# Performance work log

Hardware: AMD Instinct MI355X
Metric: run time of the kernel (lower is better)

The kernel has to match this reference:

```python
import jax, jax.numpy as jnp
import numpy as np

EPS_LN1 = 1e-6   # partial(nn.LayerNorm, eps=1e-6)
EPS_OUT = 1e-5   # nn.LayerNorm default inside SS3D out_norm


def _layernorm(x, w, b, eps):
    m = jnp.mean(x, axis=-1, keepdims=True)
    v = jnp.var(x, axis=-1, keepdims=True)
    return (x - m) * jax.lax.rsqrt(v + eps) * w + b


def _selective_scan(dA, dBx):
    # dA, dBx: (B, K, d, L, N); linear recurrence h_t = dA_t * h_{t-1} + dBx_t
    def comb(c1, c2):
        a1, b1 = c1
        a2, b2 = c2
        return a2 * a1, a2 * b1 + b2
    _, hs = jax.lax.associative_scan(comb, (dA, dBx), axis=3)
    return hs  # (B, K, d, L, N)


def setup_inputs() -> dict:
    key = jax.random.key(0)
    ks = jax.random.split(key, 12)
    B, D, H, W, C = 1, 16, 16, 16, 96
    d, N, K, R = 96, 16, 6, 6  # d_inner, d_state, n_scan_dirs, dt_rank
    s = 0.02
    f = lambda k, shp: jax.random.normal(k, shp, dtype=jnp.float32)
    return {
        "x": f(ks[0], (B, D, H, W, C)),
        "ln1_w": jnp.ones((C,), jnp.float32),
        "ln1_b": jnp.zeros((C,), jnp.float32),
        "in_proj_w": f(ks[1], (2 * d, C)) * s,
        "conv_w": f(ks[2], (d, 1, 3, 3, 3)) * s,
        "conv_b": f(ks[3], (d,)) * s,
        "x_proj_w": f(ks[4], (K, R + 2 * N, d)) * s,
        "dt_proj_w": f(ks[5], (K, d, R)) * s,
        "dt_proj_b": f(ks[6], (K, d)) * s,
        "A_log": jnp.log(1.0 + 15.0 * jax.random.uniform(ks[7], (K, d, N), jnp.float32)),
        "D_skip": f(ks[8], (K, d)) * s,
        "out_norm_w": jnp.ones((d,), jnp.float32),
        "out_norm_b": jnp.zeros((d,), jnp.float32),
        "out_proj_w": f(ks[9], (C, d)) * s,
    }


def reference(x, ln1_w, ln1_b, in_proj_w, conv_w, conv_b, x_proj_w,
              dt_proj_w, dt_proj_b, A_log, D_skip, out_norm_w, out_norm_b,
              out_proj_w):
    B, D, H, W, C = x.shape
    L = D * H * W
    K, _, d = x_proj_w.shape
    R = dt_proj_w.shape[2]
    N = A_log.shape[2]

    # pre-norm
    xn = _layernorm(x, ln1_w, ln1_b, EPS_LN1)

    # in_proj -> (x, z)
    xz = jnp.einsum('bdhwc,ec->bdhwe', xn, in_proj_w)  # (B,D,H,W,2d)
    xh, z = jnp.split(xz, 2, axis=-1)

    # depthwise 3x3x3 conv + SiLU, channels-first
    xc = jnp.transpose(xh, (0, 4, 1, 2, 3))  # (B,d,D,H,W)
    xc = jax.lax.conv_general_dilated(
        xc, conv_w, window_strides=(1, 1, 1), padding='SAME',
        dimension_numbers=('NCDHW', 'OIDHW', 'NCDHW'),
        feature_group_count=d)
    xc = jax.nn.silu(xc + conv_b[None, :, None, None, None])

    # K = 6 scan orderings: DHW, HWD, WDH and their reverses
    o0 = xc.reshape(B, d, L)
    o1 = jnp.transpose(xc, (0, 1, 3, 4, 2)).reshape(B, d, L)  # (H,W,D) order
    o2 = jnp.transpose(xc, (0, 1, 4, 2, 3)).reshape(B, d, L)  # (W,D,H) order
    fwd3 = jnp.stack([o0, o1, o2], axis=1)                    # (B,3,d,L)
    xs = jnp.concatenate([fwd3, jnp.flip(fwd3, axis=-1)], axis=1)  # (B,K,d,L)

    # per-direction input-dependent parameters
    x_dbl = jnp.einsum('bkdl,kcd->bkcl', xs, x_proj_w)        # (B,K,R+2N,L)
    dt, Bm, Cm = jnp.split(x_dbl, [R, R + N], axis=2)
    dts = jnp.einsum('bkrl,kdr->bkdl', dt, dt_proj_w) + dt_proj_b[None, :, :, None]
    dts = jax.nn.softplus(dts)                                # delta_softplus

    A = -jnp.exp(A_log)                                       # (K,d,N)
    dA = jnp.exp(dts[..., None] * A[None, :, :, None, :])     # (B,K,d,L,N)
    Bt = jnp.transpose(Bm, (0, 1, 3, 2))                      # (B,K,L,N)
    dBx = (dts * xs)[..., None] * Bt[:, :, None, :, :]        # (B,K,d,L,N)

    hs = _selective_scan(dA, dBx)                             # (B,K,d,L,N)
    Ct = jnp.transpose(Cm, (0, 1, 3, 2))                      # (B,K,L,N)
    ys = jnp.einsum('bkdln,bkln->bkdl', hs, Ct) + D_skip[None, :, :, None] * xs

    # undo reversals and orderings, sum the 6 paths
    yf = ys[:, :3] + jnp.flip(ys[:, 3:], axis=-1)             # (B,3,d,L)
    y0 = yf[:, 0]
    y1 = jnp.transpose(yf[:, 1].reshape(B, d, H, W, D), (0, 1, 4, 2, 3)).reshape(B, d, L)
    y2 = jnp.transpose(yf[:, 2].reshape(B, d, W, D, H), (0, 1, 3, 4, 2)).reshape(B, d, L)
    y = (y0 + y1 + y2).reshape(B, d, D, H, W)
    y = jnp.transpose(y, (0, 2, 3, 4, 1))                     # (B,D,H,W,d)

    # out_norm, gate, out_proj
    y = _layernorm(y, out_norm_w, out_norm_b, EPS_OUT)
    y = y * jax.nn.silu(z)
    out = jnp.einsum('bdhwe,ce->bdhwc', y, out_proj_w)

    # residual (drop_path is identity at eval)
    return x + out
```

## Files before the change

kernel.cpp:

```cpp
#include <hip/hip_runtime.h>
#include <hip/hip_bf16.h>

#define L 4096
#define CDIM 96
#define DDIM 96
#define KDIR 6
#define NST 16
#define RRK 6
#define YH 32
#define NCHUNK 256
#define CHLEN 16

typedef _Float16 half4v __attribute__((ext_vector_type(4)));

__device__ __forceinline__ float sigmoidf_(float x) { return 1.f / (1.f + __expf(-x)); }

__device__ __forceinline__ int sigma_k(int kb, int l) {
    if (kb == 0) return l;
    if (kb == 1) return ((l & 15) << 8) | ((l >> 8) << 4) | ((l >> 4) & 15);
    return (((l >> 4) & 15) << 8) | ((l & 15) << 4) | (l >> 8);
}

__device__ __forceinline__ int lrow_k(int k, int s) {
    int kb = (k < 3) ? k : (k - 3);
    int l;
    if (kb == 0) l = s;
    else if (kb == 1) l = sigma_k(2, s);
    else l = sigma_k(1, s);
    return (k >= 3) ? (4095 - l) : l;
}

__global__ void __launch_bounds__(192) k1_ln_inproj(
        const float* __restrict__ x, const float* __restrict__ ln_w,
        const float* __restrict__ ln_b, const float* __restrict__ Wp,
        _Float16* __restrict__ xhh, _Float16* __restrict__ zsh) {
    int s0 = blockIdx.x * 8;
    int tid = threadIdx.x;
    __shared__ __align__(16) float xt[8][96];
    __shared__ __align__(16) float xn[8][96];
    __shared__ float mss[8], rss[8];
    ((float4*)&xt[0][0])[tid] = ((const float4*)(x + (size_t)s0 * 96))[tid];
    __syncthreads();
    int wave = tid >> 6, lane = tid & 63;
    for (int r = wave; r < 8; r += 3) {
        float v = xt[r][lane] + ((lane < 32) ? xt[r][64 + lane] : 0.f);
#pragma unroll
        for (int off = 1; off < 64; off <<= 1) v += __shfl_xor(v, off);
        float vs = xt[r][lane] * xt[r][lane] + ((lane < 32) ? xt[r][64 + lane] * xt[r][64 + lane] : 0.f);
#pragma unroll
        for (int off = 1; off < 64; off <<= 1) vs += __shfl_xor(vs, off);
        if (lane == 0) {
            float mean = v * (1.f / 96.f);
            float var = vs * (1.f / 96.f) - mean * mean;
            mss[r] = mean; rss[r] = rsqrtf(var + 1e-6f);
        }
    }
    __syncthreads();
    {
        int r = tid / 24, c4 = tid % 24;
        float4 xv = ((float4*)&xt[r][0])[c4];
        float4 wv = ((const float4*)ln_w)[c4];
        float4 bv = ((const float4*)ln_b)[c4];
        float m = mss[r], rs = rss[r];
        float4 o;
        o.x = (xv.x - m) * rs * wv.x + bv.x;
        o.y = (xv.y - m) * rs * wv.y + bv.y;
        o.z = (xv.z - m) * rs * wv.z + bv.z;
        o.w = (xv.w - m) * rs * wv.w + bv.w;
        ((float4*)&xn[r][0])[c4] = o;
    }
    float4 Wr[24];
    const float4* wr = (const float4*)(Wp + (size_t)tid * 96);
#pragma unroll
    for (int c4 = 0; c4 < 24; c4++) Wr[c4] = wr[c4];
    __syncthreads();
#pragma unroll
    for (int s = 0; s < 8; s++) {
        const float4* xr4 = (const float4*)&xn[s][0];
        float a0 = 0.f, a1 = 0.f, a2 = 0.f, a3 = 0.f;
#pragma unroll
        for (int c4 = 0; c4 < 24; c4 += 4) {
            float4 x0 = xr4[c4], x1 = xr4[c4 + 1], x2 = xr4[c4 + 2], x3 = xr4[c4 + 3];
            a0 += Wr[c4].x * x0.x + Wr[c4].y * x0.y + Wr[c4].z * x0.z + Wr[c4].w * x0.w;
            a1 += Wr[c4+1].x * x1.x + Wr[c4+1].y * x1.y + Wr[c4+1].z * x1.z + Wr[c4+1].w * x1.w;
            a2 += Wr[c4+2].x * x2.x + Wr[c4+2].y * x2.y + Wr[c4+2].z * x2.z + Wr[c4+2].w * x2.w;
            a3 += Wr[c4+3].x * x3.x + Wr[c4+3].y * x3.y + Wr[c4+3].z * x3.z + Wr[c4+3].w * x3.w;
        }
        float acc = (a0 + a1) + (a2 + a3);
        if (tid < 96) xhh[(size_t)tid * L + s0 + s] = (_Float16)acc;
        else zsh[(size_t)(s0 + s) * 96 + (tid - 96)] = (_Float16)(acc * sigmoidf_(acc));
    }
}

__global__ void k2_conv(const _Float16* __restrict__ xhh, const float* __restrict__ cw,
                        const float* __restrict__ cb, _Float16* __restrict__ xch,
                        _Float16* __restrict__ xcTh) {
    int idx = blockIdx.x * 256 + threadIdx.x;
    int c = idx >> 12, s = idx & 4095;
    int dz = s >> 8, h = (s >> 4) & 15, w = s & 15;
    const _Float16* xin = xhh + (size_t)c * L;
    const float* wc = cw + c * 27;
    float acc = cb[c];
#pragma unroll
    for (int i = 0; i < 3; i++) {
        int z2 = dz + i - 1; if ((unsigned)z2 > 15u) continue;
#pragma unroll
        for (int j = 0; j < 3; j++) {
            int h2 = h + j - 1; if ((unsigned)h2 > 15u) continue;
#pragma unroll
            for (int kk = 0; kk < 3; kk++) {
                int w2 = w + kk - 1; if ((unsigned)w2 > 15u) continue;
                acc += (float)xin[z2 * 256 + h2 * 16 + w2] * wc[i * 9 + j * 3 + kk];
            }
        }
    }
    float r = acc * sigmoidf_(acc);
    _Float16 hr = (_Float16)r;
    xch[(size_t)c * L + s] = hr;
    xcTh[(size_t)s * 96 + c] = hr;
}

__global__ void k3_xproj(const _Float16* __restrict__ xch, const float* __restrict__ Wx,
                         const float* __restrict__ Wdt, const float* __restrict__ bdt,
                         _Float16* __restrict__ Yl, _Float16* __restrict__ Zl,
                         _Float16* __restrict__ dtxl) {
    int k = blockIdx.x;
    int tid = threadIdx.x;
    int sbase = blockIdx.y * 256;
    int s = sbase + tid;
    int g = blockIdx.z;
    __shared__ float dts[256][6];
    __shared__ _Float16 xcs[96][258];
    float acc[14];
#pragma unroll
    for (int i = 0; i < 14; i++) acc[i] = 0.f;
    const float* wdt_rows = Wx + (size_t)k * 38 * DDIM;
    const float* wbc      = Wx + ((size_t)k * 38 + 6 + g * 8) * DDIM;
    for (int dd = 0; dd < 96; dd += 4) {
        float v[4];
#pragma unroll
        for (int j = 0; j < 4; j++) {
            _Float16 hv = xch[(size_t)(dd + j) * L + s];
            v[j] = (float)hv;
            xcs[dd + j][tid] = hv;
        }
#pragma unroll
        for (int j = 0; j < 4; j++) {
#pragma unroll
            for (int r = 0; r < 6; r++) acc[r] += wdt_rows[r * DDIM + dd + j] * v[j];
#pragma unroll
            for (int i = 0; i < 8; i++) acc[6 + i] += wbc[i * DDIM + dd + j] * v[j];
        }
    }
    {
        int lr = lrow_k(k, s);
        _Float16* yo = Yl + ((size_t)k * L + lr) * YH;
#pragma unroll
        for (int i = 0; i < 8; i++) yo[g * 8 + i] = (_Float16)acc[6 + i];
    }
#pragma unroll
    for (int r = 0; r < 6; r++) dts[tid][r] = acc[r];
    __syncthreads();
    for (int i = 0; i < 24; i++) {
        int idx = i * 256 + tid;
        int dl = idx % 24;
        int sr = idx / 24;
        int d = g * 24 + dl;
        const float* wr = Wdt + ((size_t)k * 96 + d) * 6;
        float a = bdt[k * 96 + d];
#pragma unroll
        for (int r = 0; r < 6; r++) a += wr[r] * dts[sr][r];
        float sp = (a > 15.f) ? a : __logf(1.f + __expf(a));
        int lr = lrow_k(k, sbase + sr);
        size_t o = ((size_t)k * L + lr) * 96 + d;
        Zl[o] = (_Float16)sp;
        dtxl[o] = (_Float16)(sp * (float)xcs[d][sr]);
    }
}

__global__ void __launch_bounds__(256) ka_scan(
        const _Float16* __restrict__ Zl, const _Float16* __restrict__ dtxl,
        const _Float16* __restrict__ Yl, const float* __restrict__ A_log,
        _Float16* __restrict__ Aah, _Float16* __restrict__ Abh) {
    int t = blockIdx.x * 256 + threadIdx.x;
    int nq = t & 3;
    int q = t >> 2;
    int d = q % 96;
    int rest = q / 96;
    int chunk = rest % NCHUNK;
    int k = rest / NCHUNK;
    float An[4];
    {
        float4 al = *(const float4*)(A_log + ((size_t)k * 96 + d) * 16 + nq * 4);
        An[0] = -__expf(al.x) * 1.44269504f; An[1] = -__expf(al.y) * 1.44269504f;
        An[2] = -__expf(al.z) * 1.44269504f; An[3] = -__expf(al.w) * 1.44269504f;
    }
    float a[4] = {1.f, 1.f, 1.f, 1.f};
    float b[4] = {0.f, 0.f, 0.f, 0.f};
    const _Float16* Zk = Zl + (size_t)k * L * 96;
    const _Float16* Xk = dtxl + (size_t)k * L * 96;
    const _Float16* Yk = Yl + (size_t)k * L * YH;
    int l0 = chunk * CHLEN;
    for (int i = 0; i < CHLEN; i += 4) {
        float dt[4], dx[4]; half4v Bh[4];
#pragma unroll
        for (int j = 0; j < 4; j++) {
            int l = l0 + i + j;
            dt[j] = (float)Zk[(size_t)l * 96 + d];
            dx[j] = (float)Xk[(size_t)l * 96 + d];
            Bh[j] = *(const half4v*)(Yk + (size_t)l * YH + nq * 4);
        }
#pragma unroll
        for (int j = 0; j < 4; j++) {
            float e0 = exp2f(dt[j] * An[0]);
            float e1 = exp2f(dt[j] * An[1]);
            float e2 = exp2f(dt[j] * An[2]);
            float e3 = exp2f(dt[j] * An[3]);
            b[0] = e0 * b[0] + dx[j] * (float)Bh[j].x; a[0] *= e0;
            b[1] = e1 * b[1] + dx[j] * (float)Bh[j].y; a[1] *= e1;
            b[2] = e2 * b[2] + dx[j] * (float)Bh[j].z; a[2] *= e2;
            b[3] = e3 * b[3] + dx[j] * (float)Bh[j].w; a[3] *= e3;
        }
    }
    size_t o = (((size_t)k * NCHUNK + chunk) * 96 + d) * 16 + nq * 4;
    half4v ha, hb;
    ha.x = (_Float16)a[0]; ha.y = (_Float16)a[1]; ha.z = (_Float16)a[2]; ha.w = (_Float16)a[3];
    hb.x = (_Float16)b[0]; hb.y = (_Float16)b[1]; hb.z = (_Float16)b[2]; hb.w = (_Float16)b[3];
    *(half4v*)(Aah + o) = ha;
    *(half4v*)(Abh + o) = hb;
}

__global__ void __launch_bounds__(256) kb_combine(
        const _Float16* __restrict__ Aah, const _Float16* __restrict__ Abh,
        _Float16* __restrict__ Pbh) {
    int t = blockIdx.x * 256 + threadIdx.x;
    int n = t & 15;
    int rest = t >> 4;
    int d = rest % 96;
    int k = rest / 96;
    size_t base = ((size_t)k * NCHUNK * 96 + d) * 16 + n;
    const size_t cstride = 96 * 16;
    float rb = 0.f;
    for (int c0 = 0; c0 < NCHUNK; c0 += 16) {
        float av[16], bv[16];
#pragma unroll
        for (int j = 0; j < 16; j++) {
            av[j] = (float)Aah[base + (size_t)(c0 + j) * cstride];
            bv[j] = (float)Abh[base + (size_t)(c0 + j) * cstride];
        }
#pragma unroll
        for (int j = 0; j < 16; j++) {
            Pbh[base + (size_t)(c0 + j) * cstride] = (_Float16)rb;
            rb = av[j] * rb + bv[j];
        }
    }
}

__global__ void __launch_bounds__(256) kc_apply(
        const _Float16* __restrict__ Zl, const _Float16* __restrict__ dtxl,
        const _Float16* __restrict__ Yl, const float* __restrict__ A_log,
        const _Float16* __restrict__ Pbh, _Float16* __restrict__ ysh) {
    int t = blockIdx.x * 256 + threadIdx.x;
    int nq = t & 3;
    int q = t >> 2;
    int d = q % 96;
    int rest = q / 96;
    int chunk = rest % NCHUNK;
    int k = rest / NCHUNK;
    int kb = (k < 3) ? k : (k - 3);
    bool flip = (k >= 3);
    float An[4];
    {
        float4 al = *(const float4*)(A_log + ((size_t)k * 96 + d) * 16 + nq * 4);
        An[0] = -__expf(al.x) * 1.44269504f; An[1] = -__expf(al.y) * 1.44269504f;
        An[2] = -__expf(al.z) * 1.44269504f; An[3] = -__expf(al.w) * 1.44269504f;
    }
    float h[4];
    {
        half4v hp = *(const half4v*)(Pbh + (((size_t)k * NCHUNK + chunk) * 96 + d) * 16 + nq * 4);
        h[0] = (float)hp.x; h[1] = (float)hp.y; h[2] = (float)hp.z; h[3] = (float)hp.w;
    }
    const _Float16* Zk = Zl + (size_t)k * L * 96;
    const _Float16* Xk = dtxl + (size_t)k * L * 96;
    const _Float16* Yk = Yl + (size_t)k * L * YH;
    int l0 = chunk * CHLEN;
    for (int i = 0; i < CHLEN; i += 4) {
        float dt[4], dx[4]; half4v Bh[4], Ch[4];
#pragma unroll
        for (int j = 0; j < 4; j++) {
            int l = l0 + i + j;
            dt[j] = (float)Zk[(size_t)l * 96 + d];
            dx[j] = (float)Xk[(size_t)l * 96 + d];
            Bh[j] = *(const half4v*)(Yk + (size_t)l * YH + nq * 4);
            Ch[j] = *(const half4v*)(Yk + (size_t)l * YH + 16 + nq * 4);
        }
#pragma unroll
        for (int j = 0; j < 4; j++) {
            int l = l0 + i + j;
            float e0 = exp2f(dt[j] * An[0]);
            float e1 = exp2f(dt[j] * An[1]);
            float e2 = exp2f(dt[j] * An[2]);
            float e3 = exp2f(dt[j] * An[3]);
            h[0] = e0 * h[0] + dx[j] * (float)Bh[j].x;
            h[1] = e1 * h[1] + dx[j] * (float)Bh[j].y;
            h[2] = e2 * h[2] + dx[j] * (float)Bh[j].z;
            h[3] = e3 * h[3] + dx[j] * (float)Bh[j].w;
            float p = h[0] * (float)Ch[j].x + h[1] * (float)Ch[j].y
                    + h[2] * (float)Ch[j].z + h[3] * (float)Ch[j].w;
            p += __shfl_xor(p, 1);
            p += __shfl_xor(p, 2);
            if (nq == 0) {
                int lp = flip ? (4095 - l) : l;
                int sI = sigma_k(kb, lp);
                ysh[((size_t)sI * KDIR + k) * 96 + d] = (_Float16)p;
            }
        }
    }
}

__global__ void __launch_bounds__(192) k6_out(
        const _Float16* __restrict__ ysh, const _Float16* __restrict__ zsh,
        const _Float16* __restrict__ xcTh, const float* __restrict__ D_skip,
        const float* __restrict__ onw, const float* __restrict__ onb,
        const float* __restrict__ Wo, const float* __restrict__ x,
        float* __restrict__ out) {
    int s0 = blockIdx.x * 8;
    int tid = threadIdx.x;
    __shared__ __align__(16) float vt[8][96];
    __shared__ __align__(16) float gt[8][96];
    __shared__ float mss[8], rss[8];
#pragma unroll
    for (int j = 0; j < 4; j++) {
        int f = tid + j * 192;
        int sr = f / 96, c = f % 96;
        const _Float16* yr = ysh + ((size_t)(s0 + sr) * KDIR) * 96 + c;
        float v = 0.f;
#pragma unroll
        for (int k = 0; k < KDIR; k++) v += (float)yr[k * 96];
        float ds = 0.f;
#pragma unroll
        for (int k = 0; k < KDIR; k++) ds += D_skip[k * DDIM + c];
        v += ds * (float)xcTh[(size_t)(s0 + sr) * 96 + c];
        vt[sr][c] = v;
    }
    __syncthreads();
    int wave = tid >> 6, lane = tid & 63;
    for (int r = wave; r < 8; r += 3) {
        float v = vt[r][lane] + ((lane < 32) ? vt[r][64 + lane] : 0.f);
#pragma unroll
        for (int off = 1; off < 64; off <<= 1) v += __shfl_xor(v, off);
        float vs = vt[r][lane] * vt[r][lane] + ((lane < 32) ? vt[r][64 + lane] * vt[r][64 + lane] : 0.f);
#pragma unroll
        for (int off = 1; off < 64; off <<= 1) vs += __shfl_xor(vs, off);
        if (lane == 0) {
            float mean = v * (1.f / 96.f);
            float var = vs * (1.f / 96.f) - mean * mean;
            mss[r] = mean; rss[r] = rsqrtf(var + 1e-5f);
        }
    }
    __syncthreads();
#pragma unroll
    for (int j = 0; j < 4; j++) {
        int f = tid + j * 192;
        int sr = f / 96, c = f % 96;
        float g = (vt[sr][c] - mss[sr]) * rss[sr] * onw[c] + onb[c];
        gt[sr][c] = g * (float)zsh[(size_t)(s0 + sr) * 96 + c];
    }
    int e = tid % 96, sg = tid / 96;
    float4 Wr[24];
    const float4* wr = (const float4*)(Wo + (size_t)e * 96);
#pragma unroll
    for (int c4 = 0; c4 < 24; c4++) Wr[c4] = wr[c4];
    __syncthreads();
#pragma unroll
    for (int j = 0; j < 4; j++) {
        int s = sg * 4 + j;
        const float4* g4 = (const float4*)&gt[s][0];
        float a0 = 0.f, a1 = 0.f, a2 = 0.f, a3 = 0.f;
#pragma unroll
        for (int c4 = 0; c4 < 24; c4 += 4) {
            float4 x0 = g4[c4], x1 = g4[c4 + 1], x2 = g4[c4 + 2], x3 = g4[c4 + 3];
            a0 += Wr[c4].x * x0.x + Wr[c4].y * x0.y + Wr[c4].z * x0.z + Wr[c4].w * x0.w;
            a1 += Wr[c4+1].x * x1.x + Wr[c4+1].y * x1.y + Wr[c4+1].z * x1.z + Wr[c4+1].w * x1.w;
            a2 += Wr[c4+2].x * x2.x + Wr[c4+2].y * x2.y + Wr[c4+2].z * x2.z + Wr[c4+2].w * x2.w;
            a3 += Wr[c4+3].x * x3.x + Wr[c4+3].y * x3.y + Wr[c4+3].z * x3.z + Wr[c4+3].w * x3.w;
        }
        float acc = (a0 + a1) + (a2 + a3) + x[(size_t)(s0 + s) * 96 + e];
        out[(size_t)(s0 + s) * 96 + e] = acc;
    }
}

extern "C" void kernel_launch(void* const* d_in, const int* in_sizes, int n_in,
                              void* d_out, int out_size, void* d_ws, size_t ws_size,
                              hipStream_t stream) {
    const float* x        = (const float*)d_in[0];
    const float* ln1_w    = (const float*)d_in[1];
    const float* ln1_b    = (const float*)d_in[2];
    const float* in_proj  = (const float*)d_in[3];
    const float* conv_w   = (const float*)d_in[4];
    const float* conv_b   = (const float*)d_in[5];
    const float* x_proj   = (const float*)d_in[6];
    const float* dt_w     = (const float*)d_in[7];
    const float* dt_b     = (const float*)d_in[8];
    const float* A_log    = (const float*)d_in[9];
    const float* D_skip   = (const float*)d_in[10];
    const float* onw      = (const float*)d_in[11];
    const float* onb      = (const float*)d_in[12];
    const float* out_w    = (const float*)d_in[13];
    float* out = (float*)d_out;

    _Float16* xhh  = (_Float16*)d_ws;
    _Float16* zsh  = xhh + (size_t)96 * L;
    _Float16* xch  = zsh + (size_t)96 * L;
    _Float16* xcTh = xch + (size_t)96 * L;
    _Float16* Yl   = xcTh + (size_t)96 * L;
    _Float16* Zl   = Yl + (size_t)KDIR * L * YH;
    _Float16* dtxl = Zl + (size_t)KDIR * L * 96;
    _Float16* ysh  = dtxl + (size_t)KDIR * L * 96;
    _Float16* Aah  = ysh + (size_t)L * KDIR * 96;
    _Float16* Abh  = Aah + (size_t)KDIR * NCHUNK * DDIM * NST;
    _Float16* Pbh  = Abh + (size_t)KDIR * NCHUNK * DDIM * NST;

    k1_ln_inproj<<<dim3(L / 8), dim3(192), 0, stream>>>(x, ln1_w, ln1_b, in_proj, xhh, zsh);
    k2_conv<<<dim3(96 * L / 256), dim3(256), 0, stream>>>(xhh, conv_w, conv_b, xch, xcTh);
    k3_xproj<<<dim3(KDIR, 16, 4), dim3(256), 0, stream>>>(xch, x_proj, dt_w, dt_b, Yl, Zl, dtxl);
    ka_scan<<<dim3(KDIR * NCHUNK * DDIM * 4 / 256), dim3(256), 0, stream>>>(Zl, dtxl, Yl, A_log, Aah, Abh);
    kb_combine<<<dim3(KDIR * DDIM * NST / 256), dim3(256), 0, stream>>>(Aah, Abh, Pbh);
    kc_apply<<<dim3(KDIR * NCHUNK * DDIM * 4 / 256), dim3(256), 0, stream>>>(Zl, dtxl, Yl, A_log, Pbh, ysh);
    k6_out<<<dim3(L / 8), dim3(192), 0, stream>>>(ysh, zsh, xcTh, D_skip, onw, onb, out_w, x, out);
}
```

Measured before the change: 184.7 us.

## Fuse chunked scan phases into one cooperative kernel with grid syncs

Merges the three chunked selective-scan kernels (chunk reduce, cross-chunk combine, apply) into one cooperative kernel separated by grid-wide syncs, removing two kernel launches and the gaps between them. It halves the chunk count to 128 by doubling the chunk length to 32, so the whole scan fits in a 1152-block co-resident grid, and the serial combine phase gets shorter. It also interleaves B and C in the Yl layout so the apply phase fetches both with one 8-wide half load. A fallback to separate launches is kept if the cooperative launch fails. The risks are grid-sync overhead, the occupancy limit required for co-residency, and less parallelism per phase.

Result: slower. 451.1 us (+144.2%).

```diff
diff --git a/kernel.cpp b/kernel.cpp
--- a/kernel.cpp
+++ b/kernel.cpp
@@ -1,5 +1,8 @@
 #include <hip/hip_runtime.h>
 #include <hip/hip_bf16.h>
+#include <hip/hip_cooperative_groups.h>
+
+namespace cg = cooperative_groups;
 
 #define L 4096
 #define CDIM 96
@@ -8,10 +11,12 @@
 #define NST 16
 #define RRK 6
 #define YH 32
-#define NCHUNK 256
-#define CHLEN 16
+#define NCHUNK 128
+#define CHLEN 32
+#define SCAN_GRID 1152
 
 typedef _Float16 half4v __attribute__((ext_vector_type(4)));
+typedef _Float16 half8v __attribute__((ext_vector_type(8)));
 
 __device__ __forceinline__ float sigmoidf_(float x) { return 1.f / (1.f + __expf(-x)); }
 
@@ -156,7 +161,12 @@
         int lr = lrow_k(k, s);
         _Float16* yo = Yl + ((size_t)k * L + lr) * YH;
 #pragma unroll
-        for (int i = 0; i < 8; i++) yo[g * 8 + i] = (_Float16)acc[6 + i];
+        for (int i = 0; i < 8; i++) {
+            int oc = g * 8 + i;
+            int n = (oc < 16) ? oc : (oc - 16);
+            int pos = (n >> 2) * 8 + ((oc < 16) ? 0 : 4) + (n & 3);
+            yo[pos] = (_Float16)acc[6 + i];
+        }
     }
 #pragma unroll
     for (int r = 0; r < 6; r++) dts[tid][r] = acc[r];
@@ -178,11 +188,11 @@
     }
 }
 
-__global__ void __launch_bounds__(256) ka_scan(
-        const _Float16* __restrict__ Zl, const _Float16* __restrict__ dtxl,
+
+__device__ __forceinline__ void scan_phaseA(
+        int t, const _Float16* __restrict__ Zl, const _Float16* __restrict__ dtxl,
         const _Float16* __restrict__ Yl, const float* __restrict__ A_log,
         _Float16* __restrict__ Aah, _Float16* __restrict__ Abh) {
-    int t = blockIdx.x * 256 + threadIdx.x;
     int nq = t & 3;
     int q = t >> 2;
     int d = q % 96;
@@ -208,7 +218,7 @@
             int l = l0 + i + j;
             dt[j] = (float)Zk[(size_t)l * 96 + d];
             dx[j] = (float)Xk[(size_t)l * 96 + d];
-            Bh[j] = *(const half4v*)(Yk + (size_t)l * YH + nq * 4);
+            Bh[j] = *(const half4v*)(Yk + (size_t)l * YH + nq * 8);
         }
 #pragma unroll
         for (int j = 0; j < 4; j++) {
@@ -216,24 +226,23 @@
             float e1 = exp2f(dt[j] * An[1]);
             float e2 = exp2f(dt[j] * An[2]);
             float e3 = exp2f(dt[j] * An[3]);
-            b[0] = e0 * b[0] + dx[j] * (float)Bh[j].x; a[0] *= e0;
-            b[1] = e1 * b[1] + dx[j] * (float)Bh[j].y; a[1] *= e1;
-            b[2] = e2 * b[2] + dx[j] * (float)Bh[j].z; a[2] *= e2;
-            b[3] = e3 * b[3] + dx[j] * (float)Bh[j].w; a[3] *= e3;
+            b[0] = e0 * b[0] + dx[j] * (float)Bh[j][0]; a[0] *= e0;
+            b[1] = e1 * b[1] + dx[j] * (float)Bh[j][1]; a[1] *= e1;
+            b[2] = e2 * b[2] + dx[j] * (float)Bh[j][2]; a[2] *= e2;
+            b[3] = e3 * b[3] + dx[j] * (float)Bh[j][3]; a[3] *= e3;
         }
     }
     size_t o = (((size_t)k * NCHUNK + chunk) * 96 + d) * 16 + nq * 4;
     half4v ha, hb;
-    ha.x = (_Float16)a[0]; ha.y = (_Float16)a[1]; ha.z = (_Float16)a[2]; ha.w = (_Float16)a[3];
-    hb.x = (_Float16)b[0]; hb.y = (_Float16)b[1]; hb.z = (_Float16)b[2]; hb.w = (_Float16)b[3];
+    ha[0] = (_Float16)a[0]; ha[1] = (_Float16)a[1]; ha[2] = (_Float16)a[2]; ha[3] = (_Float16)a[3];
+    hb[0] = (_Float16)b[0]; hb[1] = (_Float16)b[1]; hb[2] = (_Float16)b[2]; hb[3] = (_Float16)b[3];
     *(half4v*)(Aah + o) = ha;
     *(half4v*)(Abh + o) = hb;
 }
 
-__global__ void __launch_bounds__(256) kb_combine(
-        const _Float16* __restrict__ Aah, const _Float16* __restrict__ Abh,
+__device__ __forceinline__ void scan_phaseB(
+        int t, const _Float16* __restrict__ Aah, const _Float16* __restrict__ Abh,
         _Float16* __restrict__ Pbh) {
-    int t = blockIdx.x * 256 + threadIdx.x;
     int n = t & 15;
     int rest = t >> 4;
     int d = rest % 96;
@@ -256,11 +265,10 @@
     }
 }
 
-__global__ void __launch_bounds__(256) kc_apply(
-        const _Float16* __restrict__ Zl, const _Float16* __restrict__ dtxl,
+__device__ __forceinline__ void scan_phaseC(
+        int t, const _Float16* __restrict__ Zl, const _Float16* __restrict__ dtxl,
         const _Float16* __restrict__ Yl, const float* __restrict__ A_log,
         const _Float16* __restrict__ Pbh, _Float16* __restrict__ ysh) {
-    int t = blockIdx.x * 256 + threadIdx.x;
     int nq = t & 3;
     int q = t >> 2;
     int d = q % 96;
@@ -278,21 +286,20 @@
     float h[4];
     {
         half4v hp = *(const half4v*)(Pbh + (((size_t)k * NCHUNK + chunk) * 96 + d) * 16 + nq * 4);
-        h[0] = (float)hp.x; h[1] = (float)hp.y; h[2] = (float)hp.z; h[3] = (float)hp.w;
+        h[0] = (float)hp[0]; h[1] = (float)hp[1]; h[2] = (float)hp[2]; h[3] = (float)hp[3];
     }
     const _Float16* Zk = Zl + (size_t)k * L * 96;
     const _Float16* Xk = dtxl + (size_t)k * L * 96;
     const _Float16* Yk = Yl + (size_t)k * L * YH;
     int l0 = chunk * CHLEN;
     for (int i = 0; i < CHLEN; i += 4) {
-        float dt[4], dx[4]; half4v Bh[4], Ch[4];
+        float dt[4], dx[4]; half8v Vh[4];
 #pragma unroll
         for (int j = 0; j < 4; j++) {
             int l = l0 + i + j;
             dt[j] = (float)Zk[(size_t)l * 96 + d];
             dx[j] = (float)Xk[(size_t)l * 96 + d];
-            Bh[j] = *(const half4v*)(Yk + (size_t)l * YH + nq * 4);
-            Ch[j] = *(const half4v*)(Yk + (size_t)l * YH + 16 + nq * 4);
+            Vh[j] = *(const half8v*)(Yk + (size_t)l * YH + nq * 8);
         }
 #pragma unroll
         for (int j = 0; j < 4; j++) {
@@ -301,12 +308,12 @@
             float e1 = exp2f(dt[j] * An[1]);
             float e2 = exp2f(dt[j] * An[2]);
             float e3 = exp2f(dt[j] * An[3]);
-            h[0] = e0 * h[0] + dx[j] * (float)Bh[j].x;
-            h[1] = e1 * h[1] + dx[j] * (float)Bh[j].y;
-            h[2] = e2 * h[2] + dx[j] * (float)Bh[j].z;
-            h[3] = e3 * h[3] + dx[j] * (float)Bh[j].w;
-            float p = h[0] * (float)Ch[j].x + h[1] * (float)Ch[j].y
-                    + h[2] * (float)Ch[j].z + h[3] * (float)Ch[j].w;
+            h[0] = e0 * h[0] + dx[j] * (float)Vh[j][0];
+            h[1] = e1 * h[1] + dx[j] * (float)Vh[j][1];
+            h[2] = e2 * h[2] + dx[j] * (float)Vh[j][2];
+            h[3] = e3 * h[3] + dx[j] * (float)Vh[j][3];
+            float p = h[0] * (float)Vh[j][4] + h[1] * (float)Vh[j][5]
+                    + h[2] * (float)Vh[j][6] + h[3] * (float)Vh[j][7];
             p += __shfl_xor(p, 1);
             p += __shfl_xor(p, 2);
             if (nq == 0) {
@@ -316,6 +323,38 @@
             }
         }
     }
+}
+
+__global__ void __launch_bounds__(256, 5) kscan3(
+        const _Float16* __restrict__ Zl, const _Float16* __restrict__ dtxl,
+        const _Float16* __restrict__ Yl, const float* __restrict__ A_log,
+        _Float16* __restrict__ Aah, _Float16* __restrict__ Abh,
+        _Float16* __restrict__ Pbh, _Float16* __restrict__ ysh) {
+    cg::grid_group grid = cg::this_grid();
+    int t = blockIdx.x * 256 + threadIdx.x;
+    scan_phaseA(t, Zl, dtxl, Yl, A_log, Aah, Abh);
+    grid.sync();
+    if (t < KDIR * DDIM * NST) scan_phaseB(t, Aah, Abh, Pbh);
+    grid.sync();
+    scan_phaseC(t, Zl, dtxl, Yl, A_log, Pbh, ysh);
+}
+
+__global__ void __launch_bounds__(256) ka_scan(
+        const _Float16* __restrict__ Zl, const _Float16* __restrict__ dtxl,
+        const _Float16* __restrict__ Yl, const float* __restrict__ A_log,
+        _Float16* __restrict__ Aah, _Float16* __restrict__ Abh) {
+    scan_phaseA(blockIdx.x * 256 + threadIdx.x, Zl, dtxl, Yl, A_log, Aah, Abh);
+}
+__global__ void __launch_bounds__(256) kb_combine(
+        const _Float16* __restrict__ Aah, const _Float16* __restrict__ Abh,
+        _Float16* __restrict__ Pbh) {
+    scan_phaseB(blockIdx.x * 256 + threadIdx.x, Aah, Abh, Pbh);
+}
+__global__ void __launch_bounds__(256) kc_apply(
+        const _Float16* __restrict__ Zl, const _Float16* __restrict__ dtxl,
+        const _Float16* __restrict__ Yl, const float* __restrict__ A_log,
+        const _Float16* __restrict__ Pbh, _Float16* __restrict__ ysh) {
+    scan_phaseC(blockIdx.x * 256 + threadIdx.x, Zl, dtxl, Yl, A_log, Pbh, ysh);
 }
 
 __global__ void __launch_bounds__(192) k6_out(
@@ -424,8 +463,19 @@
     k1_ln_inproj<<<dim3(L / 8), dim3(192), 0, stream>>>(x, ln1_w, ln1_b, in_proj, xhh, zsh);
     k2_conv<<<dim3(96 * L / 256), dim3(256), 0, stream>>>(xhh, conv_w, conv_b, xch, xcTh);
     k3_xproj<<<dim3(KDIR, 16, 4), dim3(256), 0, stream>>>(xch, x_proj, dt_w, dt_b, Yl, Zl, dtxl);
-    ka_scan<<<dim3(KDIR * NCHUNK * DDIM * 4 / 256), dim3(256), 0, stream>>>(Zl, dtxl, Yl, A_log, Aah, Abh);
-    kb_combine<<<dim3(KDIR * DDIM * NST / 256), dim3(256), 0, stream>>>(Aah, Abh, Pbh);
-    kc_apply<<<dim3(KDIR * NCHUNK * DDIM * 4 / 256), dim3(256), 0, stream>>>(Zl, dtxl, Yl, A_log, Pbh, ysh);
+
+    void* args[] = {
+        (void*)&Zl, (void*)&dtxl, (void*)&Yl, (void*)&A_log,
+        (void*)&Aah, (void*)&Abh, (void*)&Pbh, (void*)&ysh
+    };
+    hipError_t err = hipLaunchCooperativeKernel(kscan3, dim3(SCAN_GRID), dim3(256),
+                                                args, 0u, stream);
+    if (err != hipSuccess) {
+        (void)hipGetLastError();
+        ka_scan<<<dim3(SCAN_GRID), dim3(256), 0, stream>>>(Zl, dtxl, Yl, A_log, Aah, Abh);
+        kb_combine<<<dim3(KDIR * DDIM * NST / 256), dim3(256), 0, stream>>>(Aah, Abh, Pbh);
+        kc_apply<<<dim3(SCAN_GRID), dim3(256), 0, stream>>>(Zl, dtxl, Yl, A_log, Pbh, ysh);
+    }
+
     k6_out<<<dim3(L / 8), dim3(192), 0, stream>>>(ysh, zsh, xcTh, D_skip, onw, onb, out_w, x, out);
 }
```

## Store scan intermediates in fp32 with interleaved dt/dtx and B/C layouts

Applied to the files above, without the earlier changes.

Switches the selective-scan intermediates (dt, dt*x, B, C, chunk carries) from fp16 to fp32. It interleaves dt with dt*x into float2 pairs and B with C into per-quad float4 groups, so each thread does fewer, wider loads. The intent is better vector loads and fewer conversions, and likely better accuracy too. The cost is roughly twice the workspace traffic across k3, the scan kernels and the combine kernel.

Result: slower. 190.1 us (+2.9%).

```diff
diff --git a/kernel.cpp b/kernel.cpp
--- a/kernel.cpp
+++ b/kernel.cpp
@@ -7,7 +7,7 @@
 #define KDIR 6
 #define NST 16
 #define RRK 6
-#define YH 32
+#define YW 32
 #define NCHUNK 256
 #define CHLEN 16
 
@@ -122,8 +122,7 @@
 
 __global__ void k3_xproj(const _Float16* __restrict__ xch, const float* __restrict__ Wx,
                          const float* __restrict__ Wdt, const float* __restrict__ bdt,
-                         _Float16* __restrict__ Yl, _Float16* __restrict__ Zl,
-                         _Float16* __restrict__ dtxl) {
+                         float* __restrict__ Ylf, float* __restrict__ zxl) {
     int k = blockIdx.x;
     int tid = threadIdx.x;
     int sbase = blockIdx.y * 256;
@@ -154,9 +153,14 @@
     }
     {
         int lr = lrow_k(k, s);
-        _Float16* yo = Yl + ((size_t)k * L + lr) * YH;
-#pragma unroll
-        for (int i = 0; i < 8; i++) yo[g * 8 + i] = (_Float16)acc[6 + i];
+        float* yo = Ylf + ((size_t)k * L + lr) * YW;
+#pragma unroll
+        for (int i = 0; i < 8; i++) {
+            int oc = g * 8 + i;
+            int n = (oc < 16) ? oc : (oc - 16);
+            int pos = (n >> 2) * 8 + ((oc < 16) ? 0 : 4) + (n & 3);
+            yo[pos] = acc[6 + i];
+        }
     }
 #pragma unroll
     for (int r = 0; r < 6; r++) dts[tid][r] = acc[r];
@@ -173,15 +177,15 @@
         float sp = (a > 15.f) ? a : __logf(1.f + __expf(a));
         int lr = lrow_k(k, sbase + sr);
         size_t o = ((size_t)k * L + lr) * 96 + d;
-        Zl[o] = (_Float16)sp;
-        dtxl[o] = (_Float16)(sp * (float)xcs[d][sr]);
+        float2 zz; zz.x = sp; zz.y = sp * (float)xcs[d][sr];
+        *(float2*)(zxl + o * 2) = zz;
     }
 }
 
 __global__ void __launch_bounds__(256) ka_scan(
-        const _Float16* __restrict__ Zl, const _Float16* __restrict__ dtxl,
-        const _Float16* __restrict__ Yl, const float* __restrict__ A_log,
-        _Float16* __restrict__ Aah, _Float16* __restrict__ Abh) {
+        const float* __restrict__ zxl, const float* __restrict__ Ylf,
+        const float* __restrict__ A_log,
+        float* __restrict__ Aaf, float* __restrict__ Abf) {
     int t = blockIdx.x * 256 + threadIdx.x;
     int nq = t & 3;
     int q = t >> 2;
@@ -197,42 +201,40 @@
     }
     float a[4] = {1.f, 1.f, 1.f, 1.f};
     float b[4] = {0.f, 0.f, 0.f, 0.f};
-    const _Float16* Zk = Zl + (size_t)k * L * 96;
-    const _Float16* Xk = dtxl + (size_t)k * L * 96;
-    const _Float16* Yk = Yl + (size_t)k * L * YH;
+    const float* ZXk = zxl + (size_t)k * L * 96 * 2;
+    const float* Yk  = Ylf + (size_t)k * L * YW;
     int l0 = chunk * CHLEN;
     for (int i = 0; i < CHLEN; i += 4) {
-        float dt[4], dx[4]; half4v Bh[4];
+        float2 zx[4]; float4 Bv[4];
 #pragma unroll
         for (int j = 0; j < 4; j++) {
             int l = l0 + i + j;
-            dt[j] = (float)Zk[(size_t)l * 96 + d];
-            dx[j] = (float)Xk[(size_t)l * 96 + d];
-            Bh[j] = *(const half4v*)(Yk + (size_t)l * YH + nq * 4);
-        }
-#pragma unroll
-        for (int j = 0; j < 4; j++) {
-            float e0 = exp2f(dt[j] * An[0]);
-            float e1 = exp2f(dt[j] * An[1]);
-            float e2 = exp2f(dt[j] * An[2]);
-            float e3 = exp2f(dt[j] * An[3]);
-            b[0] = e0 * b[0] + dx[j] * (float)Bh[j].x; a[0] *= e0;
-            b[1] = e1 * b[1] + dx[j] * (float)Bh[j].y; a[1] *= e1;
-            b[2] = e2 * b[2] + dx[j] * (float)Bh[j].z; a[2] *= e2;
-            b[3] = e3 * b[3] + dx[j] * (float)Bh[j].w; a[3] *= e3;
+            zx[j] = *(const float2*)(ZXk + ((size_t)l * 96 + d) * 2);
+            Bv[j] = *(const float4*)(Yk + (size_t)l * YW + nq * 8);
+        }
+#pragma unroll
+        for (int j = 0; j < 4; j++) {
+            float e0 = exp2f(zx[j].x * An[0]);
+            float e1 = exp2f(zx[j].x * An[1]);
+            float e2 = exp2f(zx[j].x * An[2]);
+            float e3 = exp2f(zx[j].x * An[3]);
+            b[0] = e0 * b[0] + zx[j].y * Bv[j].x; a[0] *= e0;
+            b[1] = e1 * b[1] + zx[j].y * Bv[j].y; a[1] *= e1;
+            b[2] = e2 * b[2] + zx[j].y * Bv[j].z; a[2] *= e2;
+            b[3] = e3 * b[3] + zx[j].y * Bv[j].w; a[3] *= e3;
         }
     }
     size_t o = (((size_t)k * NCHUNK + chunk) * 96 + d) * 16 + nq * 4;
-    half4v ha, hb;
-    ha.x = (_Float16)a[0]; ha.y = (_Float16)a[1]; ha.z = (_Float16)a[2]; ha.w = (_Float16)a[3];
-    hb.x = (_Float16)b[0]; hb.y = (_Float16)b[1]; hb.z = (_Float16)b[2]; hb.w = (_Float16)b[3];
-    *(half4v*)(Aah + o) = ha;
-    *(half4v*)(Abh + o) = hb;
+    float4 fa, fb;
+    fa.x = a[0]; fa.y = a[1]; fa.z = a[2]; fa.w = a[3];
+    fb.x = b[0]; fb.y = b[1]; fb.z = b[2]; fb.w = b[3];
+    *(float4*)(Aaf + o) = fa;
+    *(float4*)(Abf + o) = fb;
 }
 
 __global__ void __launch_bounds__(256) kb_combine(
-        const _Float16* __restrict__ Aah, const _Float16* __restrict__ Abh,
-        _Float16* __restrict__ Pbh) {
+        const float* __restrict__ Aaf, const float* __restrict__ Abf,
+        float* __restrict__ Pbf) {
     int t = blockIdx.x * 256 + threadIdx.x;
     int n = t & 15;
     int rest = t >> 4;
@@ -245,21 +247,21 @@
         float av[16], bv[16];
 #pragma unroll
         for (int j = 0; j < 16; j++) {
-            av[j] = (float)Aah[base + (size_t)(c0 + j) * cstride];
-            bv[j] = (float)Abh[base + (size_t)(c0 + j) * cstride];
+            av[j] = Aaf[base + (size_t)(c0 + j) * cstride];
+            bv[j] = Abf[base + (size_t)(c0 + j) * cstride];
         }
 #pragma unroll
         for (int j = 0; j < 16; j++) {
-            Pbh[base + (size_t)(c0 + j) * cstride] = (_Float16)rb;
+            Pbf[base + (size_t)(c0 + j) * cstride] = rb;
             rb = av[j] * rb + bv[j];
         }
     }
 }
 
 __global__ void __launch_bounds__(256) kc_apply(
-        const _Float16* __restrict__ Zl, const _Float16* __restrict__ dtxl,
-        const _Float16* __restrict__ Yl, const float* __restrict__ A_log,
-        const _Float16* __restrict__ Pbh, _Float16* __restrict__ ysh) {
+        const float* __restrict__ zxl, const float* __restrict__ Ylf,
+        const float* __restrict__ A_log, const float* __restrict__ Pbf,
+        _Float16* __restrict__ ysh) {
     int t = blockIdx.x * 256 + threadIdx.x;
     int nq = t & 3;
     int q = t >> 2;
@@ -277,36 +279,33 @@
     }
     float h[4];
     {
-        half4v hp = *(const half4v*)(Pbh + (((size_t)k * NCHUNK + chunk) * 96 + d) * 16 + nq * 4);
-        h[0] = (float)hp.x; h[1] = (float)hp.y; h[2] = (float)hp.z; h[3] = (float)hp.w;
-    }
-    const _Float16* Zk = Zl + (size_t)k * L * 96;
-    const _Float16* Xk = dtxl + (size_t)k * L * 96;
-    const _Float16* Yk = Yl + (size_t)k * L * YH;
+        float4 hp = *(const float4*)(Pbf + (((size_t)k * NCHUNK + chunk) * 96 + d) * 16 + nq * 4);
+        h[0] = hp.x; h[1] = hp.y; h[2] = hp.z; h[3] = hp.w;
+    }
+    const float* ZXk = zxl + (size_t)k * L * 96 * 2;
+    const float* Yk  = Ylf + (size_t)k * L * YW;
     int l0 = chunk * CHLEN;
     for (int i = 0; i < CHLEN; i += 4) {
-        float dt[4], dx[4]; half4v Bh[4], Ch[4];
+        float2 zx[4]; float4 Bv[4], Cv[4];
 #pragma unroll
         for (int j = 0; j < 4; j++) {
             int l = l0 + i + j;
-            dt[j] = (float)Zk[(size_t)l * 96 + d];
-            dx[j] = (float)Xk[(size_t)l * 96 + d];
-            Bh[j] = *(const half4v*)(Yk + (size_t)l * YH + nq * 4);
-            Ch[j] = *(const half4v*)(Yk + (size_t)l * YH + 16 + nq * 4);
+            zx[j] = *(const float2*)(ZXk + ((size_t)l * 96 + d) * 2);
+            Bv[j] = *(const float4*)(Yk + (size_t)l * YW + nq * 8);
+            Cv[j] = *(const float4*)(Yk + (size_t)l * YW + nq * 8 + 4);
         }
 #pragma unroll
         for (int j = 0; j < 4; j++) {
             int l = l0 + i + j;
-            float e0 = exp2f(dt[j] * An[0]);
-            float e1 = exp2f(dt[j] * An[1]);
-            float e2 = exp2f(dt[j] * An[2]);
-            float e3 = exp2f(dt[j] * An[3]);
-            h[0] = e0 * h[0] + dx[j] * (float)Bh[j].x;
-            h[1] = e1 * h[1] + dx[j] * (float)Bh[j].y;
-            h[2] = e2 * h[2] + dx[j] * (float)Bh[j].z;
-            h[3] = e3 * h[3] + dx[j] * (float)Bh[j].w;
-            float p = h[0] * (float)Ch[j].x + h[1] * (float)Ch[j].y
-                    + h[2] * (float)Ch[j].z + h[3] * (float)Ch[j].w;
+            float e0 = exp2f(zx[j].x * An[0]);
+            float e1 = exp2f(zx[j].x * An[1]);
+            float e2 = exp2f(zx[j].x * An[2]);
+            float e3 = exp2f(zx[j].x * An[3]);
+            h[0] = e0 * h[0] + zx[j].y * Bv[j].x;
+            h[1] = e1 * h[1] + zx[j].y * Bv[j].y;
+            h[2] = e2 * h[2] + zx[j].y * Bv[j].z;
+            h[3] = e3 * h[3] + zx[j].y * Bv[j].w;
+            float p = h[0] * Cv[j].x + h[1] * Cv[j].y + h[2] * Cv[j].z + h[3] * Cv[j].w;
             p += __shfl_xor(p, 1);
             p += __shfl_xor(p, 2);
             if (nq == 0) {
@@ -409,23 +408,22 @@
     const float* out_w    = (const float*)d_in[13];
     float* out = (float*)d_out;
 
-    _Float16* xhh  = (_Float16*)d_ws;
+    float* Ylf = (float*)d_ws;
+    float* zxl = Ylf + (size_t)KDIR * L * YW;
+    float* Aaf = zxl + (size_t)KDIR * L * 96 * 2;
+    float* Abf = Aaf + (size_t)KDIR * NCHUNK * DDIM * NST;
+    float* Pbf = Abf + (size_t)KDIR * NCHUNK * DDIM * NST;
+    _Float16* xhh  = (_Float16*)(Pbf + (size_t)KDIR * NCHUNK * DDIM * NST);
     _Float16* zsh  = xhh + (size_t)96 * L;
     _Float16* xch  = zsh + (size_t)96 * L;
     _Float16* xcTh = xch + (size_t)96 * L;
-    _Float16* Yl   = xcTh + (size_t)96 * L;
-    _Float16* Zl   = Yl + (size_t)KDIR * L * YH;
-    _Float16* dtxl = Zl + (size_t)KDIR * L * 96;
-    _Float16* ysh  = dtxl + (size_t)KDIR * L * 96;
-    _Float16* Aah  = ysh + (size_t)L * KDIR * 96;
-    _Float16* Abh  = Aah + (size_t)KDIR * NCHUNK * DDIM * NST;
-    _Float16* Pbh  = Abh + (size_t)KDIR * NCHUNK * DDIM * NST;
+    _Float16* ysh  = xcTh + (size_t)96 * L;
 
     k1_ln_inproj<<<dim3(L / 8), dim3(192), 0, stream>>>(x, ln1_w, ln1_b, in_proj, xhh, zsh);
     k2_conv<<<dim3(96 * L / 256), dim3(256), 0, stream>>>(xhh, conv_w, conv_b, xch, xcTh);
-    k3_xproj<<<dim3(KDIR, 16, 4), dim3(256), 0, stream>>>(xch, x_proj, dt_w, dt_b, Yl, Zl, dtxl);
-    ka_scan<<<dim3(KDIR * NCHUNK * DDIM * 4 / 256), dim3(256), 0, stream>>>(Zl, dtxl, Yl, A_log, Aah, Abh);
-    kb_combine<<<dim3(KDIR * DDIM * NST / 256), dim3(256), 0, stream>>>(Aah, Abh, Pbh);
-    kc_apply<<<dim3(KDIR * NCHUNK * DDIM * 4 / 256), dim3(256), 0, stream>>>(Zl, dtxl, Yl, A_log, Pbh, ysh);
+    k3_xproj<<<dim3(KDIR, 16, 4), dim3(256), 0, stream>>>(xch, x_proj, dt_w, dt_b, Ylf, zxl);
+    ka_scan<<<dim3(KDIR * NCHUNK * DDIM * 4 / 256), dim3(256), 0, stream>>>(zxl, Ylf, A_log, Aaf, Abf);
+    kb_combine<<<dim3(KDIR * DDIM * NST / 256), dim3(256), 0, stream>>>(Aaf, Abf, Pbf);
+    kc_apply<<<dim3(KDIR * NCHUNK * DDIM * 4 / 256), dim3(256), 0, stream>>>(zxl, Ylf, A_log, Pbf, ysh);
     k6_out<<<dim3(L / 8), dim3(192), 0, stream>>>(ysh, zsh, xcTh, D_skip, onw, onb, out_w, x, out);
 }
```

## Interleave dt/dtx and B/C buffers; compute chunk decay from summed dt

Applied to the files above, without the earlier changes.

Stores softplus dt and dt*x interleaved as half2 pairs, and interleaves B and C per state quad so the apply kernel fetches both with one 16-byte load. The scan kernel now keeps a running sum of dt and computes the chunk's cumulative decay with one exp2 per state at the end, instead of multiplying the decays step by step. This cuts the number of load instructions and multiplies in the scan kernels. The trade-off is that the k3 writes become scattered half2 stores and the dt sum is slightly different numerically.

Result: no change. 186.8 us (+1.1%).

```diff
diff --git a/kernel.cpp b/kernel.cpp
--- a/kernel.cpp
+++ b/kernel.cpp
@@ -7,11 +7,13 @@
 #define KDIR 6
 #define NST 16
 #define RRK 6
-#define YH 32
+#define YW 32
 #define NCHUNK 256
 #define CHLEN 16
 
+typedef _Float16 half2v __attribute__((ext_vector_type(2)));
 typedef _Float16 half4v __attribute__((ext_vector_type(4)));
+typedef _Float16 half8v __attribute__((ext_vector_type(8)));
 
 __device__ __forceinline__ float sigmoidf_(float x) { return 1.f / (1.f + __expf(-x)); }
 
@@ -122,8 +124,7 @@
 
 __global__ void k3_xproj(const _Float16* __restrict__ xch, const float* __restrict__ Wx,
                          const float* __restrict__ Wdt, const float* __restrict__ bdt,
-                         _Float16* __restrict__ Yl, _Float16* __restrict__ Zl,
-                         _Float16* __restrict__ dtxl) {
+                         _Float16* __restrict__ Ylh, _Float16* __restrict__ zxh) {
     int k = blockIdx.x;
     int tid = threadIdx.x;
     int sbase = blockIdx.y * 256;
@@ -154,9 +155,14 @@
     }
     {
         int lr = lrow_k(k, s);
-        _Float16* yo = Yl + ((size_t)k * L + lr) * YH;
-#pragma unroll
-        for (int i = 0; i < 8; i++) yo[g * 8 + i] = (_Float16)acc[6 + i];
+        _Float16* yo = Ylh + ((size_t)k * L + lr) * YW;
+#pragma unroll
+        for (int i = 0; i < 8; i++) {
+            int oc = g * 8 + i;
+            int n = (oc < 16) ? oc : (oc - 16);
+            int pos = (n >> 2) * 8 + ((oc < 16) ? 0 : 4) + (n & 3);
+            yo[pos] = (_Float16)acc[6 + i];
+        }
     }
 #pragma unroll
     for (int r = 0; r < 6; r++) dts[tid][r] = acc[r];
@@ -172,15 +178,16 @@
         for (int r = 0; r < 6; r++) a += wr[r] * dts[sr][r];
         float sp = (a > 15.f) ? a : __logf(1.f + __expf(a));
         int lr = lrow_k(k, sbase + sr);
-        size_t o = ((size_t)k * L + lr) * 96 + d;
-        Zl[o] = (_Float16)sp;
-        dtxl[o] = (_Float16)(sp * (float)xcs[d][sr]);
+        half2v zz;
+        zz[0] = (_Float16)sp;
+        zz[1] = (_Float16)(sp * (float)xcs[d][sr]);
+        *(half2v*)(zxh + (((size_t)k * L + lr) * 96 + d) * 2) = zz;
     }
 }
 
 __global__ void __launch_bounds__(256) ka_scan(
-        const _Float16* __restrict__ Zl, const _Float16* __restrict__ dtxl,
-        const _Float16* __restrict__ Yl, const float* __restrict__ A_log,
+        const _Float16* __restrict__ zxh, const _Float16* __restrict__ Ylh,
+        const float* __restrict__ A_log,
         _Float16* __restrict__ Aah, _Float16* __restrict__ Abh) {
     int t = blockIdx.x * 256 + threadIdx.x;
     int nq = t & 3;
@@ -195,37 +202,42 @@
         An[0] = -__expf(al.x) * 1.44269504f; An[1] = -__expf(al.y) * 1.44269504f;
         An[2] = -__expf(al.z) * 1.44269504f; An[3] = -__expf(al.w) * 1.44269504f;
     }
-    float a[4] = {1.f, 1.f, 1.f, 1.f};
+    float dtsum = 0.f;
     float b[4] = {0.f, 0.f, 0.f, 0.f};
-    const _Float16* Zk = Zl + (size_t)k * L * 96;
-    const _Float16* Xk = dtxl + (size_t)k * L * 96;
-    const _Float16* Yk = Yl + (size_t)k * L * YH;
+    const _Float16* ZXk = zxh + (size_t)k * L * 192;
+    const _Float16* Yk  = Ylh + (size_t)k * L * YW;
     int l0 = chunk * CHLEN;
     for (int i = 0; i < CHLEN; i += 4) {
-        float dt[4], dx[4]; half4v Bh[4];
+        half2v zx[4]; half4v Bh[4];
 #pragma unroll
         for (int j = 0; j < 4; j++) {
             int l = l0 + i + j;
-            dt[j] = (float)Zk[(size_t)l * 96 + d];
-            dx[j] = (float)Xk[(size_t)l * 96 + d];
-            Bh[j] = *(const half4v*)(Yk + (size_t)l * YH + nq * 4);
-        }
-#pragma unroll
-        for (int j = 0; j < 4; j++) {
-            float e0 = exp2f(dt[j] * An[0]);
-            float e1 = exp2f(dt[j] * An[1]);
-            float e2 = exp2f(dt[j] * An[2]);
-            float e3 = exp2f(dt[j] * An[3]);
-            b[0] = e0 * b[0] + dx[j] * (float)Bh[j].x; a[0] *= e0;
-            b[1] = e1 * b[1] + dx[j] * (float)Bh[j].y; a[1] *= e1;
-            b[2] = e2 * b[2] + dx[j] * (float)Bh[j].z; a[2] *= e2;
-            b[3] = e3 * b[3] + dx[j] * (float)Bh[j].w; a[3] *= e3;
+            zx[j] = *(const half2v*)(ZXk + (size_t)l * 192 + d * 2);
+            Bh[j] = *(const half4v*)(Yk + (size_t)l * YW + nq * 8);
+        }
+#pragma unroll
+        for (int j = 0; j < 4; j++) {
+            float dt = (float)zx[j][0];
+            float dx = (float)zx[j][1];
+            float e0 = exp2f(dt * An[0]);
+            float e1 = exp2f(dt * An[1]);
+            float e2 = exp2f(dt * An[2]);
+            float e3 = exp2f(dt * An[3]);
+            b[0] = e0 * b[0] + dx * (float)Bh[j][0];
+            b[1] = e1 * b[1] + dx * (float)Bh[j][1];
+            b[2] = e2 * b[2] + dx * (float)Bh[j][2];
+            b[3] = e3 * b[3] + dx * (float)Bh[j][3];
+            dtsum += dt;
         }
     }
     size_t o = (((size_t)k * NCHUNK + chunk) * 96 + d) * 16 + nq * 4;
     half4v ha, hb;
-    ha.x = (_Float16)a[0]; ha.y = (_Float16)a[1]; ha.z = (_Float16)a[2]; ha.w = (_Float16)a[3];
-    hb.x = (_Float16)b[0]; hb.y = (_Float16)b[1]; hb.z = (_Float16)b[2]; hb.w = (_Float16)b[3];
+    ha[0] = (_Float16)exp2f(dtsum * An[0]);
+    ha[1] = (_Float16)exp2f(dtsum * An[1]);
+    ha[2] = (_Float16)exp2f(dtsum * An[2]);
+    ha[3] = (_Float16)exp2f(dtsum * An[3]);
+    hb[0] = (_Float16)b[0]; hb[1] = (_Float16)b[1];
+    hb[2] = (_Float16)b[2]; hb[3] = (_Float16)b[3];
     *(half4v*)(Aah + o) = ha;
     *(half4v*)(Abh + o) = hb;
 }
@@ -257,9 +269,9 @@
 }
 
 __global__ void __launch_bounds__(256) kc_apply(
-        const _Float16* __restrict__ Zl, const _Float16* __restrict__ dtxl,
-        const _Float16* __restrict__ Yl, const float* __restrict__ A_log,
-        const _Float16* __restrict__ Pbh, _Float16* __restrict__ ysh) {
+        const _Float16* __restrict__ zxh, const _Float16* __restrict__ Ylh,
+        const float* __restrict__ A_log, const _Float16* __restrict__ Pbh,
+        _Float16* __restrict__ ysh) {
     int t = blockIdx.x * 256 + threadIdx.x;
     int nq = t & 3;
     int q = t >> 2;
@@ -278,35 +290,34 @@
     float h[4];
     {
         half4v hp = *(const half4v*)(Pbh + (((size_t)k * NCHUNK + chunk) * 96 + d) * 16 + nq * 4);
-        h[0] = (float)hp.x; h[1] = (float)hp.y; h[2] = (float)hp.z; h[3] = (float)hp.w;
-    }
-    const _Float16* Zk = Zl + (size_t)k * L * 96;
-    const _Float16* Xk = dtxl + (size_t)k * L * 96;
-    const _Float16* Yk = Yl + (size_t)k * L * YH;
+        h[0] = (float)hp[0]; h[1] = (float)hp[1]; h[2] = (float)hp[2]; h[3] = (float)hp[3];
+    }
+    const _Float16* ZXk = zxh + (size_t)k * L * 192;
+    const _Float16* Yk  = Ylh + (size_t)k * L * YW;
     int l0 = chunk * CHLEN;
     for (int i = 0; i < CHLEN; i += 4) {
-        float dt[4], dx[4]; half4v Bh[4], Ch[4];
+        half2v zx[4]; half8v Vh[4];
 #pragma unroll
         for (int j = 0; j < 4; j++) {
             int l = l0 + i + j;
-            dt[j] = (float)Zk[(size_t)l * 96 + d];
-            dx[j] = (float)Xk[(size_t)l * 96 + d];
-            Bh[j] = *(const half4v*)(Yk + (size_t)l * YH + nq * 4);
-            Ch[j] = *(const half4v*)(Yk + (size_t)l * YH + 16 + nq * 4);
+            zx[j] = *(const half2v*)(ZXk + (size_t)l * 192 + d * 2);
+            Vh[j] = *(const half8v*)(Yk + (size_t)l * YW + nq * 8);
         }
 #pragma unroll
         for (int j = 0; j < 4; j++) {
             int l = l0 + i + j;
-            float e0 = exp2f(dt[j] * An[0]);
-            float e1 = exp2f(dt[j] * An[1]);
-            float e2 = exp2f(dt[j] * An[2]);
-            float e3 = exp2f(dt[j] * An[3]);
-            h[0] = e0 * h[0] + dx[j] * (float)Bh[j].x;
-            h[1] = e1 * h[1] + dx[j] * (float)Bh[j].y;
-            h[2] = e2 * h[2] + dx[j] * (float)Bh[j].z;
-            h[3] = e3 * h[3] + dx[j] * (float)Bh[j].w;
-            float p = h[0] * (float)Ch[j].x + h[1] * (float)Ch[j].y
-                    + h[2] * (float)Ch[j].z + h[3] * (float)Ch[j].w;
+            float dt = (float)zx[j][0];
+            float dx = (float)zx[j][1];
+            float e0 = exp2f(dt * An[0]);
+            float e1 = exp2f(dt * An[1]);
+            float e2 = exp2f(dt * An[2]);
+            float e3 = exp2f(dt * An[3]);
+            h[0] = e0 * h[0] + dx * (float)Vh[j][0];
+            h[1] = e1 * h[1] + dx * (float)Vh[j][1];
+            h[2] = e2 * h[2] + dx * (float)Vh[j][2];
+            h[3] = e3 * h[3] + dx * (float)Vh[j][3];
+            float p = h[0] * (float)Vh[j][4] + h[1] * (float)Vh[j][5]
+                    + h[2] * (float)Vh[j][6] + h[3] * (float)Vh[j][7];
             p += __shfl_xor(p, 1);
             p += __shfl_xor(p, 2);
             if (nq == 0) {
@@ -413,19 +424,18 @@
     _Float16* zsh  = xhh + (size_t)96 * L;
     _Float16* xch  = zsh + (size_t)96 * L;
     _Float16* xcTh = xch + (size_t)96 * L;
-    _Float16* Yl   = xcTh + (size_t)96 * L;
-    _Float16* Zl   = Yl + (size_t)KDIR * L * YH;
-    _Float16* dtxl = Zl + (size_t)KDIR * L * 96;
-    _Float16* ysh  = dtxl + (size_t)KDIR * L * 96;
+    _Float16* Ylh  = xcTh + (size_t)96 * L;
+    _Float16* zxh  = Ylh + (size_t)KDIR * L * YW;
+    _Float16* ysh  = zxh + (size_t)KDIR * L * 96 * 2;
     _Float16* Aah  = ysh + (size_t)L * KDIR * 96;
     _Float16* Abh  = Aah + (size_t)KDIR * NCHUNK * DDIM * NST;
     _Float16* Pbh  = Abh + (size_t)KDIR * NCHUNK * DDIM * NST;
 
     k1_ln_inproj<<<dim3(L / 8), dim3(192), 0, stream>>>(x, ln1_w, ln1_b, in_proj, xhh, zsh);
     k2_conv<<<dim3(96 * L / 256), dim3(256), 0, stream>>>(xhh, conv_w, conv_b, xch, xcTh);
-    k3_xproj<<<dim3(KDIR, 16, 4), dim3(256), 0, stream>>>(xch, x_proj, dt_w, dt_b, Yl, Zl, dtxl);
-    ka_scan<<<dim3(KDIR * NCHUNK * DDIM * 4 / 256), dim3(256), 0, stream>>>(Zl, dtxl, Yl, A_log, Aah, Abh);
+    k3_xproj<<<dim3(KDIR, 16, 4), dim3(256), 0, stream>>>(xch, x_proj, dt_w, dt_b, Ylh, zxh);
+    ka_scan<<<dim3(KDIR * NCHUNK * DDIM * 4 / 256), dim3(256), 0, stream>>>(zxh, Ylh, A_log, Aah, Abh);
     kb_combine<<<dim3(KDIR * DDIM * NST / 256), dim3(256), 0, stream>>>(Aah, Abh, Pbh);
-    kc_apply<<<dim3(KDIR * NCHUNK * DDIM * 4 / 256), dim3(256), 0, stream>>>(Zl, dtxl, Yl, A_log, Pbh, ysh);
+    kc_apply<<<dim3(KDIR * NCHUNK * DDIM * 4 / 256), dim3(256), 0, stream>>>(zxh, Ylh, A_log, Pbh, ysh);
     k6_out<<<dim3(L / 8), dim3(192), 0, stream>>>(ysh, zsh, xcTh, D_skip, onw, onb, out_w, x, out);
 }
```
